# Performance work log

Measured on AMD Instinct MI355X. Metric: run time of the kernel, lower is better.

Reference implementation:

```python
import jax, jax.numpy as jnp
from jax import lax
import numpy as np

NEIGHBORS = ((1, 3), (0, 2, 4), (1, 5), (0, 4, 6), (1, 3, 5, 7), (2, 4, 8), (3, 7), (4, 6, 8), (5, 7))
EDGE_SRC = np.array([s for t, ns in enumerate(NEIGHBORS) for s in ns])  # 25 edges
EDGE_DST = np.array([t for t, ns in enumerate(NEIGHBORS) for _ in ns])
NE = len(EDGE_SRC)  # 25
NG, SP = 9, 64      # num_grids, single_plane = 576 // 9
R, C_IN, C_OUT, ROI = 64, 256, 576, 14
GN_GROUPS = 36
EPS = 1e-5


def conv2d(x, w, b, stride, pad):
    y = lax.conv_general_dilated(x, w, (stride, stride), [(pad, pad), (pad, pad)],
                                 dimension_numbers=('NCHW', 'OIHW', 'NCHW'))
    return y + b[None, :, None, None]


def group_norm(x, groups, gamma, beta):
    B, C, H, W = x.shape
    xg = x.reshape(B, groups, -1)
    mu = xg.mean(-1, keepdims=True)
    var = xg.var(-1, keepdims=True)
    xn = ((xg - mu) / jnp.sqrt(var + EPS)).reshape(B, C, H, W)
    return xn * gamma[None, :, None, None] + beta[None, :, None, None]


def edge_conv(inp, dw_w, dw_b, pw_w, pw_b):
    # depthwise 5x5 (groups=SP) then pointwise 1x1
    y = lax.conv_general_dilated(inp, dw_w, (1, 1), [(2, 2), (2, 2)],
                                 dimension_numbers=('NCHW', 'OIHW', 'NCHW'),
                                 feature_group_count=SP) + dw_b[None, :, None, None]
    return jnp.einsum('bchw,oc->bohw', y, pw_w) + pw_b[None, :, None, None]


def deconv_grouped(x, w_t, b, groups):
    # torch ConvTranspose2d(k=4, s=2, p=1, groups) as lhs-dilated conv
    k, s, p = 4, 2, 1
    in_c, out_g = w_t.shape[0], w_t.shape[1]
    in_g = in_c // groups
    w = w_t.reshape(groups, in_g, out_g, k, k).transpose(0, 2, 1, 3, 4).reshape(groups * out_g, in_g, k, k)
    w = jnp.flip(w, (-2, -1))
    y = lax.conv_general_dilated(x, w, (1, 1), [(k - 1 - p, k - 1 - p)] * 2,
                                 lhs_dilation=(s, s),
                                 dimension_numbers=('NCHW', 'OIHW', 'NCHW'),
                                 feature_group_count=groups)
    return y + b[None, :, None, None]


def setup_inputs() -> dict:
    key = jax.random.key(0)
    ks = iter(jax.random.split(key, 32))
    n = lambda shape, s=0.02: jax.random.normal(next(ks), shape, jnp.float32) * s
    inp = {
        'x': jax.random.normal(next(ks), (R, C_IN, ROI, ROI), jnp.float32),
        'convs_w0': n((C_OUT, C_IN, 3, 3)),
        'convs_b0': n((C_OUT,)),
        'convs_w': n((7, C_OUT, C_OUT, 3, 3)),
        'convs_b': n((7, C_OUT)),
        'gn_gamma': jnp.ones((8, C_OUT), jnp.float32),
        'gn_beta': jnp.zeros((8, C_OUT), jnp.float32),
        'fo_dw_w': n((NE, SP, 1, 5, 5), 0.05),
        'fo_dw_b': n((NE, SP)),
        'fo_pw_w': n((NE, SP, SP), 0.05),
        'fo_pw_b': n((NE, SP)),
        'so_dw_w': n((NE, SP, 1, 5, 5), 0.05),
        'so_dw_b': n((NE, SP)),
        'so_pw_w': n((NE, SP, SP), 0.05),
        'so_pw_b': n((NE, SP)),
        'up1_w': n((C_OUT, SP, 4, 4), 0.01),
        'up1_b': jnp.zeros((C_OUT,), jnp.float32),
        'sbn1_gamma': jnp.ones((C_OUT,), jnp.float32),
        'sbn1_beta': jnp.zeros((C_OUT,), jnp.float32),
        'up2_w': n((C_OUT, 1, 4, 4), 0.01),
        'up2_b': jnp.full((NG,), -np.log(0.99 / 0.01), jnp.float32),
    }
    return inp


def reference(x, convs_w0, convs_b0, convs_w, convs_b, gn_gamma, gn_beta,
              fo_dw_w, fo_dw_b, fo_pw_w, fo_pw_b,
              so_dw_w, so_dw_b, so_pw_w, so_pw_b,
              up1_w, up1_b, sbn1_gamma, sbn1_beta, up2_w, up2_b):
    # dense conv stack: stride 2 first, then 7 stride-1 convs (GN + ReLU each)
    h = jax.nn.relu(group_norm(conv2d(x, convs_w0, convs_b0, 2, 1), GN_GROUPS, gn_gamma[0], gn_beta[0]))
    for i in range(7):
        h = jax.nn.relu(group_norm(conv2d(h, convs_w[i], convs_b[i], 1, 1),
                                   GN_GROUPS, gn_gamma[i + 1], gn_beta[i + 1]))
    B, _, Hh, Wh = h.shape  # [B, 576, 7, 7]
    xg = h.reshape(B, NG, SP, Hh, Wh).transpose(1, 0, 2, 3, 4)  # [9, B, 64, 7, 7]
    # first-order message passing over 25 grid edges
    msgs1 = jax.vmap(edge_conv)(xg[EDGE_SRC], fo_dw_w, fo_dw_b, fo_pw_w, fo_pw_b)
    first = xg + jax.ops.segment_sum(msgs1, EDGE_DST, num_segments=NG)
    # second-order message passing (sources are first-order features)
    msgs2 = jax.vmap(edge_conv)(first[EDGE_SRC], so_dw_w, so_dw_b, so_pw_w, so_pw_b)
    second = xg + jax.ops.segment_sum(msgs2, EDGE_DST, num_segments=NG)
    x2 = second.transpose(1, 0, 2, 3, 4).reshape(B, NG * SP, Hh, Wh)

    def head(t):
        t = deconv_grouped(t, up1_w, up1_b, NG)           # [B, 576, 14, 14]
        t = jax.nn.relu(group_norm(t, NG, sbn1_gamma, sbn1_beta))
        return deconv_grouped(t, up2_w, up2_b, NG)        # [B, 9, 28, 28]

    return (head(h), head(x2))
```

## Files before the change

kernel.cpp:

```cpp
#include <hip/hip_runtime.h>
#include <hip/hip_bf16.h>

#define BB 64
#define CIN 256
#define CC 576
#define NGR 9
#define SPC 64
#define HW7 49
#define HW14 196
#define HW28 784

__device__ __constant__ int EDGE_SRC_C[24] = {1,3, 0,2,4, 1,5, 0,4,6, 1,3,5,7, 2,4,8, 3,7, 4,6,8, 5,7};
__device__ __constant__ int EDGE_OFF_C[9]  = {0,2,5,7,10,14,17,19,22};
__device__ __constant__ int EDGE_CNT_C[9]  = {2,3,2,3,4,3,2,3,2};

static __device__ __forceinline__ float bf2f(__hip_bfloat16 v){ return __bfloat162float(v); }
static __device__ __forceinline__ __hip_bfloat16 f2bf(float v){ return __float2bfloat16(v); }
static __device__ __forceinline__ float ldin(const void* p, size_t i, int isbf){
  return isbf ? bf2f(((const __hip_bfloat16*)p)[i]) : ((const float*)p)[i];
}

using bfrag = __attribute__((ext_vector_type(8))) short;
using f32x4 = __attribute__((ext_vector_type(4))) float;

__global__ void detect_kernel(const unsigned short* xs, int* flag) {
  if (threadIdx.x==0 && blockIdx.x==0) {
    int plaus = 0;
    for (int i=0;i<64;i++){
      unsigned short u = xs[2*i];
      int e = (u>>7)&0xFF;
      if (e>=100 && e<=140) plaus++;
    }
    *flag = (plaus >= 40) ? 1 : 0;
  }
}

__global__ __launch_bounds__(256) void xcvt_kernel(
    const void* __restrict__ x, const int* __restrict__ flagp,
    __hip_bfloat16* __restrict__ act0) {
  const int b = blockIdx.x, icb = blockIdx.y, pxb = blockIdx.z, t = threadIdx.x;
  const int isbf = *flagp;
  __shared__ float lds[32][29];
  for (int idx=t; idx<32*28; idx+=256){
    int i = idx/28, j = idx - i*28;
    lds[i][j] = ldin(x, ((size_t)b*CIN + icb*32+i)*HW14 + pxb*28 + j, isbf);
  }
  __syncthreads();
  for (int idx=t; idx<28*32; idx+=256){
    int j = idx >> 5, i = idx & 31;
    act0[((size_t)b*HW14 + pxb*28 + j)*CIN + icb*32 + i] = f2bf(lds[i][j]);
  }
}

__global__ __launch_bounds__(256) void wcvt0_kernel(
    const void* __restrict__ w, const int* __restrict__ flagp,
    __hip_bfloat16* __restrict__ dst) {
  const int oc = blockIdx.x, t = threadIdx.x;
  const int isbf = *flagp;
  __shared__ float lds[2304];
  for (int idx=t; idx<2304; idx+=256)
    lds[idx] = ldin(w, (size_t)oc*2304 + idx, isbf);
  __syncthreads();
  for (int idx=t; idx<2304; idx+=256){
    int koff = idx >> 8, rem = idx & 255;
    int icb = rem >> 5, ici = rem & 31;
    dst[(((size_t)koff*8 + icb)*CC + oc)*32 + ici] = f2bf(lds[rem*9 + koff]);
  }
}

__global__ __launch_bounds__(256) void wcvtL_kernel(
    const void* __restrict__ w, int li, const int* __restrict__ flagp,
    __hip_bfloat16* __restrict__ dst) {
  const int oc = blockIdx.x, t = threadIdx.x;
  const int isbf = *flagp;
  __shared__ float lds[5184];
  for (int idx=t; idx<5184; idx+=256)
    lds[idx] = ldin(w, ((size_t)li*CC + oc)*5184 + idx, isbf);
  __syncthreads();
  for (int idx=t; idx<5184; idx+=256){
    int koff = idx / 576, rem = idx - koff*576;
    int icb = rem >> 5, ici = rem & 31;
    dst[(((size_t)koff*18 + icb)*CC + oc)*32 + ici] = f2bf(lds[rem*9 + koff]);
  }
}

static __device__ __forceinline__ void epilogue_gn(
    float* s_out, float* s_stats, const f32x4 (&acc)[2][2],
    int wm, int wn, int ln, int quad, int t,
    const void* bias, int bias_off,
    const void* gamma, const void* beta, int goff,
    int nbb, int isbf, int b,
    __hip_bfloat16* __restrict__ out)
{
  __syncthreads();
  #pragma unroll
  for (int nf=0; nf<2; nf++){
    int chl = wn*32 + nf*16 + ln;
    float bv = ldin(bias, (size_t)bias_off + nbb + chl, isbf);
    #pragma unroll
    for (int mf=0; mf<2; mf++){
      #pragma unroll
      for (int r=0; r<4; r++){
        int px = wm*32 + mf*16 + quad*4 + r;
        s_out[chl*65 + px] = acc[mf][nf][r] + bv;
      }
    }
  }
  __syncthreads();
  {
    int wv = t >> 6, l = t & 63;
    float s=0.f, ss=0.f;
    for (int j=l; j<784; j+=64){
      int cq = j/49, px = j - cq*49;
      float v = s_out[(wv*16+cq)*65 + px];
      s += v; ss += v*v;
    }
    #pragma unroll
    for (int o=32;o>0;o>>=1){ s+=__shfl_down(s,o); ss+=__shfl_down(ss,o); }
    if (l==0){
      float mean=s/784.f, var=ss/784.f-mean*mean;
      s_stats[wv*2]=mean; s_stats[wv*2+1]=rsqrtf(fmaxf(var,0.f)+1e-5f);
    }
  }
  __syncthreads();
  for (int idx=t; idx<392; idx+=256){
    int px = idx>>3, ck = idx&7;
    alignas(16) __hip_bfloat16 tmp[8];
    #pragma unroll
    for (int u=0;u<8;u++){
      int chl = ck*8+u;
      int gi = chl>>4;
      float ga = ldin(gamma, (size_t)goff + nbb + chl, isbf);
      float be = ldin(beta,  (size_t)goff + nbb + chl, isbf);
      float v = (s_out[chl*65+px]-s_stats[gi*2])*s_stats[gi*2+1]*ga + be;
      tmp[u] = f2bf(fmaxf(v,0.f));
    }
    *(bfrag*)(out + ((size_t)b*64+px)*CC + nbb + ck*8) = *(const bfrag*)tmp;
  }
}

__global__ __launch_bounds__(256) void conv3_v3_kernel(
    const __hip_bfloat16* __restrict__ A,
    const __hip_bfloat16* __restrict__ Wb,
    const void* __restrict__ bias, int bias_off,
    const void* __restrict__ gamma, const void* __restrict__ beta, int goff,
    const int* __restrict__ flagp,
    __hip_bfloat16* __restrict__ out) {
  const int t = threadIdx.x;
  const int l = t & 63, w = t >> 6;
  const int wm = w & 1, wn = (w >> 1) & 1;
  const int ln = l & 15, quad = l >> 4;
  const int b = blockIdx.x, nbb = blockIdx.y*32;
  const int isbf = *flagp;

  __shared__ alignas(16) char smem[8320];
  __shared__ float s_stats[4];
  __hip_bfloat16* sA0 = (__hip_bfloat16*)smem;
  __hip_bfloat16* sA1 = (__hip_bfloat16*)(smem + 4000);
  float* s_out = (float*)smem;

  if (t < 8){
    bfrag z = {0,0,0,0,0,0,0,0};
    __hip_bfloat16* sb = (t<4)? sA0 : sA1;
    *(bfrag*)(sb + 49*40 + (t&3)*8) = z;
  }

  int r0a[9], r1a[9];
  {
    int p0 = wm*32 + ln, p1 = p0+16;
    int y0=p0/7, x0=p0-y0*7, y1=p1/7, x1=p1-y1*7;
    bool v0=p0<49, v1=p1<49;
    #pragma unroll
    for (int koff=0;koff<9;koff++){
      int dy=koff/3-1, dx=koff-(koff/3)*3-1;
      int sy0=y0+dy,sx0=x0+dx, sy1=y1+dy,sx1=x1+dx;
      r0a[koff] = (v0&&sy0>=0&&sy0<7&&sx0>=0&&sx0<7)? sy0*7+sx0 : 49;
      r1a[koff] = (v1&&sy1>=0&&sy1<7&&sx1>=0&&sx1<7)? sy1*7+sx1 : 49;
    }
  }

  f32x4 acc2[2];
  acc2[0] = (f32x4){0.f,0.f,0.f,0.f};
  acc2[1] = (f32x4){0.f,0.f,0.f,0.f};

  const int px_s = t>>2, ic_s = (t&3)*8;
  const __hip_bfloat16* Abase = A + ((size_t)b*64 + px_s)*CC + ic_s;

  if (t<196) *(bfrag*)(sA0 + px_s*40 + ic_s) = *(const bfrag*)(Abase);
  __syncthreads();

  const int nidx = nbb + wn*16 + ln;
  for (int icb=0; icb<18; icb++){
    __hip_bfloat16* curb = (icb&1)? sA1 : sA0;
    if (icb<17 && t<196){
      __hip_bfloat16* nxtb = (icb&1)? sA0 : sA1;
      *(bfrag*)(nxtb + px_s*40 + ic_s) = *(const bfrag*)(Abase + (icb+1)*32);
    }
    const __hip_bfloat16* wpB = Wb + (size_t)icb*18432 + (size_t)nidx*32 + quad*8;
    #pragma unroll
    for (int koff=0;koff<9;koff++){
      bfrag a0 = *(const bfrag*)(curb + r0a[koff]*40 + quad*8);
      bfrag a1 = *(const bfrag*)(curb + r1a[koff]*40 + quad*8);
      bfrag b0 = *(const bfrag*)(wpB + (size_t)koff*331776);
      acc2[0] = __builtin_amdgcn_mfma_f32_16x16x32_bf16(a0, b0, acc2[0], 0,0,0);
      acc2[1] = __builtin_amdgcn_mfma_f32_16x16x32_bf16(a1, b0, acc2[1], 0,0,0);
    }
    __syncthreads();
  }

  {
    const int chl = wn*16 + ln;
    float bv = ldin(bias, (size_t)bias_off + nbb + chl, isbf);
    #pragma unroll
    for (int mf=0; mf<2; mf++)
      #pragma unroll
      for (int r=0;r<4;r++){
        int px = wm*32 + mf*16 + quad*4 + r;
        s_out[chl*65 + px] = acc2[mf][r] + bv;
      }
  }
  __syncthreads();
  {
    int wv = t >> 6, l2 = t & 63;
    if (wv < 2){
      float s=0.f, ss=0.f;
      for (int j=l2; j<784; j+=64){
        int cq = j/49, px = j - cq*49;
        float v = s_out[(wv*16+cq)*65 + px];
        s += v; ss += v*v;
      }
      #pragma unroll
      for (int o=32;o>0;o>>=1){ s+=__shfl_down(s,o); ss+=__shfl_down(ss,o); }
      if (l2==0){
        float mean=s/784.f, var=ss/784.f-mean*mean;
        s_stats[wv*2]=mean; s_stats[wv*2+1]=rsqrtf(fmaxf(var,0.f)+1e-5f);
      }
    }
  }
  __syncthreads();
  if (t < 196){
    int px = t>>2, ck = t&3;
    alignas(16) __hip_bfloat16 tmp[8];
    #pragma unroll
    for (int u=0;u<8;u++){
      int chl = ck*8+u;
      int gi = chl>>4;
      float ga = ldin(gamma, (size_t)goff + nbb + chl, isbf);
      float be = ldin(beta,  (size_t)goff + nbb + chl, isbf);
      float v = (s_out[chl*65+px]-s_stats[gi*2])*s_stats[gi*2+1]*ga + be;
      tmp[u] = f2bf(fmaxf(v,0.f));
    }
    *(bfrag*)(out + ((size_t)b*64+px)*CC + nbb + ck*8) = *(const bfrag*)tmp;
  }
}

__global__ __launch_bounds__(256) void conv0_fused_kernel(
    const __hip_bfloat16* __restrict__ A,
    const __hip_bfloat16* __restrict__ Wb,
    const void* __restrict__ bias,
    const void* __restrict__ gamma, const void* __restrict__ beta,
    const int* __restrict__ flagp,
    __hip_bfloat16* __restrict__ out) {
  const int t = threadIdx.x;
  const int l = t & 63, w = t >> 6;
  const int wm = w & 1, wn = w >> 1;
  const int ln = l & 15, quad = l >> 4;
  const int b = blockIdx.x, nbb = blockIdx.y*64;

  __shared__ alignas(16) __hip_bfloat16 sC[197*40];
  __shared__ alignas(16) float s_out_arr[64*65];
  __shared__ float s_stats[8];

  if (t < 4){
    bfrag z = {0,0,0,0,0,0,0,0};
    *(bfrag*)(sC + 196*40 + t*8) = z;
  }

  int yy[2], xx[2]; bool pv[2];
  #pragma unroll
  for (int mf=0; mf<2; mf++){
    int p = wm*32 + mf*16 + ln;
    pv[mf] = p<49; yy[mf]=p/7; xx[mf]=p-yy[mf]*7;
  }

  f32x4 acc[2][2];
  #pragma unroll
  for (int i=0;i<2;i++)
    #pragma unroll
    for (int j=0;j<2;j++) acc[i][j] = (f32x4){0.f,0.f,0.f,0.f};

  for (int icb=0; icb<8; icb++){
    __syncthreads();
    for (int idx=t*8; idx<6272; idx+=2048){
      int px = idx>>5, ic = idx&31;
      *(bfrag*)(sC + px*40 + ic) = *(const bfrag*)(A + ((size_t)b*196+px)*256 + icb*32 + ic);
    }
    __syncthreads();
    for (int koff=0; koff<9; koff++){
      const int dy = koff/3 - 1, dx = koff - (koff/3)*3 - 1;
      int sy0=2*yy[0]+dy, sx0=2*xx[0]+dx;
      int r0 = (pv[0]&&sy0>=0&&sy0<14&&sx0>=0&&sx0<14) ? sy0*14+sx0 : 196;
      int sy1=2*yy[1]+dy, sx1=2*xx[1]+dx;
      int r1 = (pv[1]&&sy1>=0&&sy1<14&&sx1>=0&&sx1<14) ? sy1*14+sx1 : 196;
      bfrag a0 = *(const bfrag*)(sC + r0*40 + quad*8);
      bfrag a1 = *(const bfrag*)(sC + r1*40 + quad*8);
      const __hip_bfloat16* wp = Wb + ((size_t)(koff*8+icb)*576 + nbb + wn*32 + ln)*32 + quad*8;
      bfrag b0 = *(const bfrag*)(wp);
      bfrag b1 = *(const bfrag*)(wp + 16*32);
      acc[0][0] = __builtin_amdgcn_mfma_f32_16x16x32_bf16(a0, b0, acc[0][0], 0,0,0);
      acc[1][0] = __builtin_amdgcn_mfma_f32_16x16x32_bf16(a1, b0, acc[1][0], 0,0,0);
      acc[0][1] = __builtin_amdgcn_mfma_f32_16x16x32_bf16(a0, b1, acc[0][1], 0,0,0);
      acc[1][1] = __builtin_amdgcn_mfma_f32_16x16x32_bf16(a1, b1, acc[1][1], 0,0,0);
    }
  }

  epilogue_gn(s_out_arr, s_stats, acc, wm, wn, ln, quad, t,
              bias, 0, gamma, beta, 0, nbb, *flagp, b, out);
}

__global__ __launch_bounds__(256) void dw_edge_kernel(
    const __hip_bfloat16* __restrict__ F,
    const void* __restrict__ dw_w,
    const void* __restrict__ dw_b,
    const int* __restrict__ flagp,
    __hip_bfloat16* __restrict__ Y) {
  const int b = blockIdx.x, e = blockIdx.y, t = threadIdx.x;
  const int isbf = *flagp;
  const int src = EDGE_SRC_C[e];
  __shared__ alignas(16) __hip_bfloat16 sA[50*72];
  for (int idx=t; idx<400; idx+=256){
    if (idx < 392){
      int px = idx>>3, ic = (idx&7)*8;
      *(bfrag*)(sA + px*72 + ic) = *(const bfrag*)(F + ((size_t)b*64+px)*CC + src*64 + ic);
    } else {
      bfrag z = {0,0,0,0,0,0,0,0};
      *(bfrag*)(sA + 49*72 + (idx-392)*8) = z;
    }
  }
  __syncthreads();
  const int ch = t & 63, wv = t >> 6;
  float wd[25];
  #pragma unroll
  for (int j=0;j<25;j++) wd[j] = ldin(dw_w, (size_t)e*1600 + ch*25 + j, isbf);
  float dwb = ldin(dw_b, e*64 + ch, isbf);
  for (int px=wv; px<49; px+=4){
    int oy=px/7, ox=px-oy*7;
    float a = dwb;
    #pragma unroll
    for (int u=0;u<5;u++){
      int py = oy+u-2;
      bool vy = (py>=0)&&(py<7);
      #pragma unroll
      for (int v=0;v<5;v++){
        int pxx = ox+v-2;
        int r = (vy && pxx>=0 && pxx<7) ? py*7+pxx : 49;
        a += bf2f(sA[r*72 + ch]) * wd[u*5+v];
      }
    }
    Y[((size_t)(e*64+b)*49 + px)*64 + ch] = f2bf(a);
  }
}

__global__ __launch_bounds__(256) void pwpack_kernel(
    const void* __restrict__ pw_fo, const void* __restrict__ pw_so,
    const int* __restrict__ flagp,
    __hip_bfloat16* __restrict__ dfo, __hip_bfloat16* __restrict__ dso) {
  const int e = blockIdx.x, t = threadIdx.x;
  const int isbf = *flagp;
  for (int idx=t; idx<4096; idx+=256){
    dfo[(size_t)e*4096+idx] = f2bf(ldin(pw_fo, (size_t)e*4096+idx, isbf));
    dso[(size_t)e*4096+idx] = f2bf(ldin(pw_so, (size_t)e*4096+idx, isbf));
  }
}

__global__ __launch_bounds__(256) void pw_seg_kernel(
    const __hip_bfloat16* __restrict__ Y,
    const __hip_bfloat16* __restrict__ base,
    const __hip_bfloat16* __restrict__ pwb,
    const void* __restrict__ pw_b,
    const int* __restrict__ flagp,
    __hip_bfloat16* __restrict__ out) {
  const int t = threadIdx.x, l = t & 63, w = t >> 6;
  const int wm = w & 1, wn = w >> 1;
  const int ln = l & 15, quad = l >> 4;
  const int dst = blockIdx.y;
  const int mt = blockIdx.x*64 + wm*32;
  const int m0 = mt + ln, m1 = m0 + 16;

  f32x4 acc[2][2];
  #pragma unroll
  for (int i=0;i<2;i++)
    #pragma unroll
    for (int j=0;j<2;j++) acc[i][j] = (f32x4){0.f,0.f,0.f,0.f};

  const int eoff = EDGE_OFF_C[dst], ecnt = EDGE_CNT_C[dst];
  for (int k=0;k<ecnt;k++){
    const __hip_bfloat16* Ye = Y + (size_t)(eoff+k)*3136*64;
    const __hip_bfloat16* pe = pwb + (size_t)(eoff+k)*4096;
    #pragma unroll
    for (int ks=0; ks<2; ks++){
      const int kq = ks*32 + quad*8;
      bfrag a0 = *(const bfrag*)(Ye + (size_t)m0*64 + kq);
      bfrag a1 = *(const bfrag*)(Ye + (size_t)m1*64 + kq);
      bfrag b0 = *(const bfrag*)(pe + (wn*32+ln)*64 + kq);
      bfrag b1 = *(const bfrag*)(pe + (wn*32+ln+16)*64 + kq);
      acc[0][0] = __builtin_amdgcn_mfma_f32_16x16x32_bf16(a0, b0, acc[0][0], 0,0,0);
      acc[1][0] = __builtin_amdgcn_mfma_f32_16x16x32_bf16(a1, b0, acc[1][0], 0,0,0);
      acc[0][1] = __builtin_amdgcn_mfma_f32_16x16x32_bf16(a0, b1, acc[0][1], 0,0,0);
      acc[1][1] = __builtin_amdgcn_mfma_f32_16x16x32_bf16(a1, b1, acc[1][1], 0,0,0);
    }
  }

  const int isbf = *flagp;
  #pragma unroll
  for (int nf=0; nf<2; nf++){
    int n = wn*32 + nf*16 + ln;
    float pbs = 0.f;
    for (int k=0;k<ecnt;k++) pbs += ldin(pw_b, (size_t)(eoff+k)*64 + n, isbf);
    #pragma unroll
    for (int mf=0; mf<2; mf++){
      #pragma unroll
      for (int r=0; r<4; r++){
        int m = mt + mf*16 + quad*4 + r;
        int bb = m/49, px = m - bb*49;
        size_t oi = ((size_t)bb*64 + px)*CC + dst*64 + n;
        out[oi] = f2bf(bf2f(base[oi]) + acc[mf][nf][r] + pbs);
      }
    }
  }
}

__global__ __launch_bounds__(256) void wpack_dc1_kernel(
    const void* __restrict__ w1, const int* __restrict__ flagp,
    __hip_bfloat16* __restrict__ dst) {
  const int gtap = blockIdx.x, t = threadIdx.x;
  const int isbf = *flagp;
  const int g = gtap >> 4, tap = gtap & 15;
  for (int idx=t; idx<64*64; idx+=256){
    int oc = idx >> 6, ic = idx & 63;
    dst[((size_t)gtap*64 + oc)*64 + ic] =
        f2bf(ldin(w1, ((size_t)(g*64+ic)*64 + oc)*16 + tap, isbf));
  }
}

__global__ __launch_bounds__(256) void dc1_cls_kernel(
    const __hip_bfloat16* __restrict__ H,
    const __hip_bfloat16* __restrict__ Wp,
    const void* __restrict__ b1,
    const int* __restrict__ flagp,
    __hip_bfloat16* __restrict__ mid) {
  const int t = threadIdx.x;
  const int l = t & 63, w = t >> 6;
  const int wm = w & 1, wn = w >> 1;
  const int ln = l & 15, quad = l >> 4;
  const int Mt = blockIdx.x;
  const int cls = blockIdx.y;
  const int g = blockIdx.z;
  const int ry = cls >> 1, rx = cls & 1;
  const int b0 = (Mt*64)/49;

  __shared__ alignas(16) __hip_bfloat16 sX[3*50*72];

  {
    const bfrag z = {0,0,0,0,0,0,0,0};
    for (int idx=t; idx<1200; idx+=256){
      int bi = idx/400, rem = idx - bi*400;
      int p = rem>>3, ch = (rem&7)*8;
      bfrag v = z;
      if (p < 49 && (b0+bi) < 64)
        v = *(const bfrag*)(H + ((size_t)((b0+bi)*64) + p)*CC + g*64 + ch);
      *(bfrag*)(sX + (bi*50+p)*72 + ch) = v;
    }
  }

  int aoff[2][4];
  #pragma unroll
  for (int mf=0; mf<2; mf++){
    int m = Mt*64 + wm*32 + mf*16 + ln;
    int b = m/49, p = m - b*49;
    int py = p/7, pxx = p - py*7;
    int bloc = b - b0;
    #pragma unroll
    for (int kyi=0;kyi<2;kyi++){
      int iy = py + ry - kyi;
      bool vy = (iy>=0)&&(iy<7);
      #pragma unroll
      for (int kxi=0;kxi<2;kxi++){
        int ix = pxx + rx - kxi;
        int r = (vy && ix>=0 && ix<7) ? iy*7+ix : 49;
        aoff[mf][kyi*2+kxi] = (bloc*50 + r)*72 + quad*8;
      }
    }
  }

  f32x4 acc[2][2];
  #pragma unroll
  for (int i=0;i<2;i++)
    #pragma unroll
    for (int j=0;j<2;j++) acc[i][j] = (f32x4){0.f,0.f,0.f,0.f};

  __syncthreads();

  const int ky0 = 1-ry, kx0 = 1-rx;
  #pragma unroll
  for (int kyi=0;kyi<2;kyi++){
    #pragma unroll
    for (int kxi=0;kxi<2;kxi++){
      const int tap = (ky0+2*kyi)*4 + (kx0+2*kxi);
      const __hip_bfloat16* wb =
          Wp + ((size_t)(g*16+tap)*64 + wn*32 + ln)*64 + quad*8;
      const int ao0 = aoff[0][kyi*2+kxi], ao1 = aoff[1][kyi*2+kxi];
      #pragma unroll
      for (int half=0; half<2; half++){
        bfrag a0 = *(const bfrag*)(sX + ao0 + half*32);
        bfrag a1 = *(const bfrag*)(sX + ao1 + half*32);
        bfrag w0 = *(const bfrag*)(wb + half*32);
        bfrag w1 = *(const bfrag*)(wb + 16*64 + half*32);
        acc[0][0] = __builtin_amdgcn_mfma_f32_16x16x32_bf16(a0, w0, acc[0][0], 0,0,0);
        acc[1][0] = __builtin_amdgcn_mfma_f32_16x16x32_bf16(a1, w0, acc[1][0], 0,0,0);
        acc[0][1] = __builtin_amdgcn_mfma_f32_16x16x32_bf16(a0, w1, acc[0][1], 0,0,0);
        acc[1][1] = __builtin_amdgcn_mfma_f32_16x16x32_bf16(a1, w1, acc[1][1], 0,0,0);
      }
    }
  }

  const int isbf = *flagp;
  size_t ob[2][4];
  #pragma unroll
  for (int mf=0;mf<2;mf++){
    #pragma unroll
    for (int r=0;r<4;r++){
      int m = Mt*64 + wm*32 + mf*16 + quad*4 + r;
      int b = m/49, p = m - b*49;
      int py = p/7, pxx = p - py*7;
      int oy = 2*py + ry, ox = 2*pxx + rx;
      ob[mf][r] = ((size_t)b*196 + oy*14 + ox)*CC + g*64;
    }
  }
  #pragma unroll
  for (int nf=0;nf<2;nf++){
    int n = wn*32 + nf*16 + ln;
    float bv = ldin(b1, g*64 + n, isbf);
    #pragma unroll
    for (int mf=0;mf<2;mf++){
      #pragma unroll
      for (int r=0;r<4;r++)
        mid[ob[mf][r] + n] = f2bf(acc[mf][nf][r] + bv);
    }
  }
}

__global__ __launch_bounds__(256) void dc2gn_kernel(
    const __hip_bfloat16* __restrict__ mid,
    const void* __restrict__ gamma, const void* __restrict__ beta,
    const void* __restrict__ w2,
    const void* __restrict__ b2,
    const int* __restrict__ flagp,
    void* __restrict__ outp,
    size_t out_elem_off) {
  const int isbf = *flagp;
  const int b=blockIdx.x, g=blockIdx.y, z=blockIdx.z, t=threadIdx.x;
  const int c = t & 63;
  __shared__ __hip_bfloat16 s_mid[64*113];
  __shared__ float s_w2[64][17];
  __shared__ float red[8]; __shared__ float stats[2];
  const __hip_bfloat16* mbase = mid + (size_t)b*196*CC + g*64;

  {
    float s=0.f, ss=0.f;
    for (int idx=t; idx<12544; idx+=256){
      int ipx = idx>>6;
      float v = bf2f(mbase[(size_t)ipx*CC + (idx&63)]);
      s+=v; ss+=v*v;
    }
    #pragma unroll
    for (int o=32;o>0;o>>=1){ s+=__shfl_down(s,o); ss+=__shfl_down(ss,o); }
    int wid=t>>6;
    if ((t&63)==0){ red[wid]=s; red[4+wid]=ss; }
  }
  for (int idx=t; idx<1024; idx+=256)
    s_w2[idx>>4][idx&15] = ldin(w2, (g*SPC + (idx>>4))*16 + (idx&15), isbf);
  __syncthreads();
  if (t==0){
    float S=red[0]+red[1]+red[2]+red[3];
    float SS=red[4]+red[5]+red[6]+red[7];
    float mean=S/12544.f, var=SS/12544.f-mean*mean;
    stats[0]=mean; stats[1]=rsqrtf(fmaxf(var,0.f)+1e-5f);
  }
  __syncthreads();
  const float mean=stats[0], inv=stats[1];
  const int rbase = z*6;
  {
    float ga = ldin(gamma, g*SPC+c, isbf), be = ldin(beta, g*SPC+c, isbf);
    for (int idx=t; idx<7168; idx+=256){
      int pl = idx>>6;
      int ipx = (rbase + pl/14)*14 + (pl%14);
      float v = (bf2f(mbase[(size_t)ipx*CC + c])-mean)*inv*ga + be;
      s_mid[c*113 + pl] = f2bf(fmaxf(v, 0.f));
    }
  }
  __syncthreads();
  float b2v = ldin(b2, g, isbf);
  for (int p=t; p<392; p+=256){
    int oyl = p/28, ox = p - oyl*28;
    int oy = z*14 + oyl;
    float a = b2v;
    for (int cc=0; cc<64; cc++){
      #pragma unroll
      for (int kyi=0;kyi<2;kyi++){
        int ky=((oy+1)&1)+2*kyi; int ny=oy+1-ky;
        if (ny>=0){
          int iy=ny>>1;
          if (iy<14){
            int li = iy - rbase;
            #pragma unroll
            for (int kxi=0;kxi<2;kxi++){
              int kx=((ox+1)&1)+2*kxi; int nx=ox+1-kx;
              if (nx>=0){
                int ix=nx>>1;
                if (ix<14) a += bf2f(s_mid[cc*113 + li*14 + ix])*s_w2[cc][ky*4+kx];
              }
            }
          }
        }
      }
    }
    size_t oidx = out_elem_off + ((size_t)b*NGR+g)*HW28 + oy*28 + ox;
    if (isbf) ((__hip_bfloat16*)outp)[oidx] = f2bf(a);
    else      ((float*)outp)[oidx] = a;
  }
}

extern "C" void kernel_launch(void* const* d_in, const int* in_sizes, int n_in,
                              void* d_out, int out_size, void* d_ws, size_t ws_size,
                              hipStream_t stream) {
  const void* x        = d_in[0];
  const void* convs_w0 = d_in[1];
  const void* convs_b0 = d_in[2];
  const void* convs_w  = d_in[3];
  const void* convs_b  = d_in[4];
  const void* gn_gamma = d_in[5];
  const void* gn_beta  = d_in[6];
  const void* fo_dw_w  = d_in[7];
  const void* fo_dw_b  = d_in[8];
  const void* fo_pw_w  = d_in[9];
  const void* fo_pw_b  = d_in[10];
  const void* so_dw_w  = d_in[11];
  const void* so_dw_b  = d_in[12];
  const void* so_pw_w  = d_in[13];
  const void* so_pw_b  = d_in[14];
  const void* up1_w    = d_in[15];
  const void* up1_b    = d_in[16];
  const void* sbn_g    = d_in[17];
  const void* sbn_b    = d_in[18];
  const void* up2_w    = d_in[19];
  const void* up2_b    = d_in[20];
  (void)in_sizes; (void)n_in; (void)out_size; (void)ws_size;

  int* flag = (int*)d_ws;
  char* wsb = (char*)d_ws + 16;
  __hip_bfloat16* act0   = (__hip_bfloat16*)(wsb);
  __hip_bfloat16* wbuf   = (__hip_bfloat16*)(wsb + 6422528);
  __hip_bfloat16* actA   = (__hip_bfloat16*)(wsb + 12394496);
  __hip_bfloat16* actB   = (__hip_bfloat16*)(wsb + 17113088);
  __hip_bfloat16* bufF   = (__hip_bfloat16*)(wsb + 21831680);
  __hip_bfloat16* secN   = (__hip_bfloat16*)(wsb + 26550272);
  __hip_bfloat16* wpack  = (__hip_bfloat16*)(wsb + 31268864);
  __hip_bfloat16* pwbF   = (__hip_bfloat16*)(wsb + 32448512);
  __hip_bfloat16* pwbS   = (__hip_bfloat16*)(wsb + 32645120);
  __hip_bfloat16* Y      = (__hip_bfloat16*)(wsb);
  __hip_bfloat16* mid    = (__hip_bfloat16*)(wsb);

  detect_kernel<<<1, 1, 0, stream>>>((const unsigned short*)x, flag);

  xcvt_kernel<<<dim3(BB,8,7), 256, 0, stream>>>(x, flag, act0);
  wcvt0_kernel<<<CC, 256, 0, stream>>>(convs_w0, flag, wbuf);
  conv0_fused_kernel<<<dim3(64,9), 256, 0, stream>>>(
      act0, wbuf, convs_b0, gn_gamma, gn_beta, flag, actA);

  __hip_bfloat16* cur = actA; __hip_bfloat16* nxt = actB;
  for (int i=0;i<7;i++){
    wcvtL_kernel<<<CC, 256, 0, stream>>>(convs_w, i, flag, wbuf);
    conv3_v3_kernel<<<dim3(64,18), 256, 0, stream>>>(
        cur, wbuf, convs_b, i*CC, gn_gamma, gn_beta, (i+1)*CC, flag, nxt);
    __hip_bfloat16* tmp=cur; cur=nxt; nxt=tmp;
  }

  wpack_dc1_kernel<<<144, 256, 0, stream>>>(up1_w, flag, wpack);
  pwpack_kernel<<<24, 256, 0, stream>>>(fo_pw_w, so_pw_w, flag, pwbF, pwbS);

  dw_edge_kernel<<<dim3(BB,24), 256, 0, stream>>>(cur, fo_dw_w, fo_dw_b, flag, Y);
  pw_seg_kernel<<<dim3(49,NGR), 256, 0, stream>>>(Y, cur, pwbF, fo_pw_b, flag, bufF);
  dw_edge_kernel<<<dim3(BB,24), 256, 0, stream>>>(bufF, so_dw_w, so_dw_b, flag, Y);
  pw_seg_kernel<<<dim3(49,NGR), 256, 0, stream>>>(Y, cur, pwbS, so_pw_b, flag, secN);

  dc1_cls_kernel<<<dim3(49,4,NGR), 256, 0, stream>>>(cur, wpack, up1_b, flag, mid);
  dc2gn_kernel<<<dim3(BB,NGR,2), 256, 0, stream>>>(mid, sbn_g, sbn_b, up2_w, up2_b, flag, d_out, 0);
  dc1_cls_kernel<<<dim3(49,4,NGR), 256, 0, stream>>>(secN, wpack, up1_b, flag, mid);
  dc2gn_kernel<<<dim3(BB,NGR,2), 256, 0, stream>>>(mid, sbn_g, sbn_b, up2_w, up2_b, flag, d_out, (size_t)BB*NGR*HW28);
}
```

Baseline: 965.9 us.

## Widen conv3 tile to 96 channels with 64-channel K steps

The 3x3 conv kernel now has each block compute 96 output channels instead of 32, with three N-fragments per wave. Each loaded A fragment is therefore reused across three MFMAs. The input-channel chunk staged in shared memory also grows from 32 to 64, halving the number of K iterations and barriers. The cost is more shared memory and accumulator registers, and the grid shrinks from 1152 to 384 blocks, which may reduce occupancy and latency hiding.

```diff
diff --git a/kernel.cpp b/kernel.cpp
--- a/kernel.cpp
+++ b/kernel.cpp
@@ -139,7 +139,7 @@
   }
 }
 
-__global__ __launch_bounds__(256) void conv3_v3_kernel(
+__global__ __launch_bounds__(256) void conv3_v4_kernel(
     const __hip_bfloat16* __restrict__ A,
     const __hip_bfloat16* __restrict__ Wb,
     const void* __restrict__ bias, int bias_off,
@@ -148,21 +148,22 @@
     __hip_bfloat16* __restrict__ out) {
   const int t = threadIdx.x;
   const int l = t & 63, w = t >> 6;
-  const int wm = w & 1, wn = (w >> 1) & 1;
+  const int wm = w & 1, wn2 = w >> 1;
   const int ln = l & 15, quad = l >> 4;
-  const int b = blockIdx.x, nbb = blockIdx.y*32;
-  const int isbf = *flagp;
-
-  __shared__ alignas(16) char smem[8320];
-  __shared__ float s_stats[4];
+  const int b = blockIdx.x, nbb = blockIdx.y*96;
+  const int isbf = *flagp;
+
+  __shared__ alignas(16) char smem[24960];
+  __shared__ float s_stats[12];
   __hip_bfloat16* sA0 = (__hip_bfloat16*)smem;
-  __hip_bfloat16* sA1 = (__hip_bfloat16*)(smem + 4000);
+  __hip_bfloat16* sA1 = (__hip_bfloat16*)(smem + 7200);
   float* s_out = (float*)smem;
 
-  if (t < 8){
+  if (t < 18){
     bfrag z = {0,0,0,0,0,0,0,0};
-    __hip_bfloat16* sb = (t<4)? sA0 : sA1;
-    *(bfrag*)(sb + 49*40 + (t&3)*8) = z;
+    __hip_bfloat16* sb = (t<9)? sA0 : sA1;
+    int c = (t<9)? t : t-9;
+    *(bfrag*)(sb + 49*72 + c*8) = z;
   }
 
   int r0a[9], r1a[9];
@@ -179,67 +180,89 @@
     }
   }
 
-  f32x4 acc2[2];
-  acc2[0] = (f32x4){0.f,0.f,0.f,0.f};
-  acc2[1] = (f32x4){0.f,0.f,0.f,0.f};
-
-  const int px_s = t>>2, ic_s = (t&3)*8;
-  const __hip_bfloat16* Abase = A + ((size_t)b*64 + px_s)*CC + ic_s;
-
-  if (t<196) *(bfrag*)(sA0 + px_s*40 + ic_s) = *(const bfrag*)(Abase);
-  __syncthreads();
-
-  const int nidx = nbb + wn*16 + ln;
-  for (int icb=0; icb<18; icb++){
+  f32x4 acc[2][3];
+  #pragma unroll
+  for (int i=0;i<2;i++)
+    #pragma unroll
+    for (int j=0;j<3;j++) acc[i][j] = (f32x4){0.f,0.f,0.f,0.f};
+
+  const __hip_bfloat16* Ab = A + (size_t)b*64*CC;
+  {
+    for (int idx=t; idx<392; idx+=256){
+      int p = idx>>3, c8 = idx&7;
+      *(bfrag*)(sA0 + p*72 + c8*8) = *(const bfrag*)(Ab + (size_t)p*CC + c8*8);
+    }
+  }
+  __syncthreads();
+
+  const int nrow = nbb + wn2*48 + ln;
+  for (int icb=0; icb<9; icb++){
     __hip_bfloat16* curb = (icb&1)? sA1 : sA0;
-    if (icb<17 && t<196){
+    if (icb<8){
       __hip_bfloat16* nxtb = (icb&1)? sA0 : sA1;
-      *(bfrag*)(nxtb + px_s*40 + ic_s) = *(const bfrag*)(Abase + (icb+1)*32);
-    }
-    const __hip_bfloat16* wpB = Wb + (size_t)icb*18432 + (size_t)nidx*32 + quad*8;
+      for (int idx=t; idx<392; idx+=256){
+        int p = idx>>3, c8 = idx&7;
+        *(bfrag*)(nxtb + p*72 + c8*8) =
+            *(const bfrag*)(Ab + (size_t)p*CC + (icb+1)*64 + c8*8);
+      }
+    }
     #pragma unroll
     for (int koff=0;koff<9;koff++){
-      bfrag a0 = *(const bfrag*)(curb + r0a[koff]*40 + quad*8);
-      bfrag a1 = *(const bfrag*)(curb + r1a[koff]*40 + quad*8);
-      bfrag b0 = *(const bfrag*)(wpB + (size_t)koff*331776);
-      acc2[0] = __builtin_amdgcn_mfma_f32_16x16x32_bf16(a0, b0, acc2[0], 0,0,0);
-      acc2[1] = __builtin_amdgcn_mfma_f32_16x16x32_bf16(a1, b0, acc2[1], 0,0,0);
+      const int ra0 = r0a[koff]*72 + quad*8;
+      const int ra1 = r1a[koff]*72 + quad*8;
+      #pragma unroll
+      for (int ks=0; ks<2; ks++){
+        const __hip_bfloat16* wp =
+            Wb + ((size_t)(koff*18 + icb*2 + ks)*576 + nrow)*32 + quad*8;
+        bfrag a0 = *(const bfrag*)(curb + ra0 + ks*32);
+        bfrag a1 = *(const bfrag*)(curb + ra1 + ks*32);
+        bfrag w0 = *(const bfrag*)(wp);
+        bfrag w1 = *(const bfrag*)(wp + 16*32);
+        bfrag w2 = *(const bfrag*)(wp + 32*32);
+        acc[0][0] = __builtin_amdgcn_mfma_f32_16x16x32_bf16(a0, w0, acc[0][0], 0,0,0);
+        acc[1][0] = __builtin_amdgcn_mfma_f32_16x16x32_bf16(a1, w0, acc[1][0], 0,0,0);
+        acc[0][1] = __builtin_amdgcn_mfma_f32_16x16x32_bf16(a0, w1, acc[0][1], 0,0,0);
+        acc[1][1] = __builtin_amdgcn_mfma_f32_16x16x32_bf16(a1, w1, acc[1][1], 0,0,0);
+        acc[0][2] = __builtin_amdgcn_mfma_f32_16x16x32_bf16(a0, w2, acc[0][2], 0,0,0);
+        acc[1][2] = __builtin_amdgcn_mfma_f32_16x16x32_bf16(a1, w2, acc[1][2], 0,0,0);
+      }
     }
     __syncthreads();
   }
 
-  {
-    const int chl = wn*16 + ln;
+  #pragma unroll
+  for (int nf=0; nf<3; nf++){
+    const int chl = wn2*48 + nf*16 + ln;
     float bv = ldin(bias, (size_t)bias_off + nbb + chl, isbf);
     #pragma unroll
     for (int mf=0; mf<2; mf++)
       #pragma unroll
       for (int r=0;r<4;r++){
         int px = wm*32 + mf*16 + quad*4 + r;
-        s_out[chl*65 + px] = acc2[mf][r] + bv;
+        s_out[chl*65 + px] = acc[mf][nf][r] + bv;
       }
   }
   __syncthreads();
   {
     int wv = t >> 6, l2 = t & 63;
-    if (wv < 2){
+    for (int g = wv; g < 6; g += 4){
       float s=0.f, ss=0.f;
       for (int j=l2; j<784; j+=64){
         int cq = j/49, px = j - cq*49;
-        float v = s_out[(wv*16+cq)*65 + px];
+        float v = s_out[(g*16+cq)*65 + px];
         s += v; ss += v*v;
       }
       #pragma unroll
       for (int o=32;o>0;o>>=1){ s+=__shfl_down(s,o); ss+=__shfl_down(ss,o); }
       if (l2==0){
         float mean=s/784.f, var=ss/784.f-mean*mean;
-        s_stats[wv*2]=mean; s_stats[wv*2+1]=rsqrtf(fmaxf(var,0.f)+1e-5f);
-      }
-    }
-  }
-  __syncthreads();
-  if (t < 196){
-    int px = t>>2, ck = t&3;
+        s_stats[g*2]=mean; s_stats[g*2+1]=rsqrtf(fmaxf(var,0.f)+1e-5f);
+      }
+    }
+  }
+  __syncthreads();
+  for (int idx=t; idx<588; idx+=256){
+    int px = idx/12, ck = idx - px*12;
     alignas(16) __hip_bfloat16 tmp[8];
     #pragma unroll
     for (int u=0;u<8;u++){
@@ -681,7 +704,7 @@
   __hip_bfloat16* cur = actA; __hip_bfloat16* nxt = actB;
   for (int i=0;i<7;i++){
     wcvtL_kernel<<<CC, 256, 0, stream>>>(convs_w, i, flag, wbuf);
-    conv3_v3_kernel<<<dim3(64,18), 256, 0, stream>>>(
+    conv3_v4_kernel<<<dim3(64,6), 256, 0, stream>>>(
         cur, wbuf, convs_b, i*CC, gn_gamma, gn_beta, (i+1)*CC, flag, nxt);
     __hip_bfloat16* tmp=cur; cur=nxt; nxt=tmp;
   }
```

Result: slower. 1.166 ms (+20.7%).

## Widen conv3x3 block tile to 64 channels with register-staged input prefetch

Applied to the files above, without the earlier changes.

The 3x3 conv+GroupNorm kernel now uses 512-thread blocks, each covering 64 output channels instead of 32. Each block also stages 64 input channels per iteration in shared memory, so the K loop has 9 steps and 9 barriers instead of 18. The next input chunk is loaded into registers before the MFMA work and written to shared memory afterwards, which hides global latency behind compute. This halves how often activations are re-read from global memory across channel blocks and cuts barrier count. The cost is a larger shared-memory footprint, fewer blocks, and more threads per block, which could reduce occupancy.

```diff
diff --git a/kernel.cpp b/kernel.cpp
--- a/kernel.cpp
+++ b/kernel.cpp
@@ -139,7 +139,7 @@
   }
 }
 
-__global__ __launch_bounds__(256) void conv3_v3_kernel(
+__global__ __launch_bounds__(512) void conv3_v5_kernel(
     const __hip_bfloat16* __restrict__ A,
     const __hip_bfloat16* __restrict__ Wb,
     const void* __restrict__ bias, int bias_off,
@@ -148,22 +148,16 @@
     __hip_bfloat16* __restrict__ out) {
   const int t = threadIdx.x;
   const int l = t & 63, w = t >> 6;
-  const int wm = w & 1, wn = (w >> 1) & 1;
+  const int wm = w & 1, wn = w >> 1;
   const int ln = l & 15, quad = l >> 4;
-  const int b = blockIdx.x, nbb = blockIdx.y*32;
-  const int isbf = *flagp;
-
-  __shared__ alignas(16) char smem[8320];
-  __shared__ float s_stats[4];
+  const int b = blockIdx.x, nbb = blockIdx.y*64;
+  const int isbf = *flagp;
+
+  __shared__ alignas(16) char smem[16672];
+  __shared__ float s_stats[8];
   __hip_bfloat16* sA0 = (__hip_bfloat16*)smem;
-  __hip_bfloat16* sA1 = (__hip_bfloat16*)(smem + 4000);
+  __hip_bfloat16* sA1 = (__hip_bfloat16*)(smem + 7200);
   float* s_out = (float*)smem;
-
-  if (t < 8){
-    bfrag z = {0,0,0,0,0,0,0,0};
-    __hip_bfloat16* sb = (t<4)? sA0 : sA1;
-    *(bfrag*)(sb + 49*40 + (t&3)*8) = z;
-  }
 
   int r0a[9], r1a[9];
   {
@@ -179,31 +173,50 @@
     }
   }
 
-  f32x4 acc2[2];
-  acc2[0] = (f32x4){0.f,0.f,0.f,0.f};
-  acc2[1] = (f32x4){0.f,0.f,0.f,0.f};
-
-  const int px_s = t>>2, ic_s = (t&3)*8;
-  const __hip_bfloat16* Abase = A + ((size_t)b*64 + px_s)*CC + ic_s;
-
-  if (t<196) *(bfrag*)(sA0 + px_s*40 + ic_s) = *(const bfrag*)(Abase);
+  f32x4 acc[2];
+  acc[0] = (f32x4){0.f,0.f,0.f,0.f};
+  acc[1] = (f32x4){0.f,0.f,0.f,0.f};
+
+  const int p_s = t>>3, c8_s = (t&7)*8;
+  const bool sact = (t < 392);
+  const __hip_bfloat16* Ab = A + (size_t)b*64*CC;
+  const __hip_bfloat16* Asrc = Ab + (size_t)p_s*CC + c8_s;
+
+  if (sact) *(bfrag*)(sA0 + p_s*72 + c8_s) = *(const bfrag*)(Asrc);
+  if (t >= 496){
+    bfrag z = {0,0,0,0,0,0,0,0};
+    int u = t - 496;
+    __hip_bfloat16* sb = (u<8)? sA0 : sA1;
+    *(bfrag*)(sb + 49*72 + (u&7)*8) = z;
+  }
   __syncthreads();
 
   const int nidx = nbb + wn*16 + ln;
-  for (int icb=0; icb<18; icb++){
+  for (int icb=0; icb<9; icb++){
     __hip_bfloat16* curb = (icb&1)? sA1 : sA0;
-    if (icb<17 && t<196){
+    bfrag rstage;
+    const bool have = (icb<8) && sact;
+    if (have) rstage = *(const bfrag*)(Asrc + (icb+1)*64);
+
+    #pragma unroll
+    for (int koff=0;koff<9;koff++){
+      const int ra0 = r0a[koff]*72 + quad*8;
+      const int ra1 = r1a[koff]*72 + quad*8;
+      #pragma unroll
+      for (int ks=0; ks<2; ks++){
+        const __hip_bfloat16* wp =
+            Wb + ((size_t)(koff*18 + icb*2 + ks)*576 + nidx)*32 + quad*8;
+        bfrag a0 = *(const bfrag*)(curb + ra0 + ks*32);
+        bfrag a1 = *(const bfrag*)(curb + ra1 + ks*32);
+        bfrag b0 = *(const bfrag*)(wp);
+        acc[0] = __builtin_amdgcn_mfma_f32_16x16x32_bf16(a0, b0, acc[0], 0,0,0);
+        acc[1] = __builtin_amdgcn_mfma_f32_16x16x32_bf16(a1, b0, acc[1], 0,0,0);
+      }
+    }
+
+    if (have){
       __hip_bfloat16* nxtb = (icb&1)? sA0 : sA1;
-      *(bfrag*)(nxtb + px_s*40 + ic_s) = *(const bfrag*)(Abase + (icb+1)*32);
-    }
-    const __hip_bfloat16* wpB = Wb + (size_t)icb*18432 + (size_t)nidx*32 + quad*8;
-    #pragma unroll
-    for (int koff=0;koff<9;koff++){
-      bfrag a0 = *(const bfrag*)(curb + r0a[koff]*40 + quad*8);
-      bfrag a1 = *(const bfrag*)(curb + r1a[koff]*40 + quad*8);
-      bfrag b0 = *(const bfrag*)(wpB + (size_t)koff*331776);
-      acc2[0] = __builtin_amdgcn_mfma_f32_16x16x32_bf16(a0, b0, acc2[0], 0,0,0);
-      acc2[1] = __builtin_amdgcn_mfma_f32_16x16x32_bf16(a1, b0, acc2[1], 0,0,0);
+      *(bfrag*)(nxtb + p_s*72 + c8_s) = rstage;
     }
     __syncthreads();
   }
@@ -216,13 +229,13 @@
       #pragma unroll
       for (int r=0;r<4;r++){
         int px = wm*32 + mf*16 + quad*4 + r;
-        s_out[chl*65 + px] = acc2[mf][r] + bv;
+        s_out[chl*65 + px] = acc[mf][r] + bv;
       }
   }
   __syncthreads();
   {
     int wv = t >> 6, l2 = t & 63;
-    if (wv < 2){
+    if (wv < 4){
       float s=0.f, ss=0.f;
       for (int j=l2; j<784; j+=64){
         int cq = j/49, px = j - cq*49;
@@ -238,8 +251,8 @@
     }
   }
   __syncthreads();
-  if (t < 196){
-    int px = t>>2, ck = t&3;
+  if (t < 392){
+    int px = t>>3, ck = t&7;
     alignas(16) __hip_bfloat16 tmp[8];
     #pragma unroll
     for (int u=0;u<8;u++){
@@ -681,7 +694,7 @@
   __hip_bfloat16* cur = actA; __hip_bfloat16* nxt = actB;
   for (int i=0;i<7;i++){
     wcvtL_kernel<<<CC, 256, 0, stream>>>(convs_w, i, flag, wbuf);
-    conv3_v3_kernel<<<dim3(64,18), 256, 0, stream>>>(
+    conv3_v5_kernel<<<dim3(64,9), 512, 0, stream>>>(
         cur, wbuf, convs_b, i*CC, gn_gamma, gn_beta, (i+1)*CC, flag, nxt);
     __hip_bfloat16* tmp=cur; cur=nxt; nxt=tmp;
   }
```

Measured after the change: 1.049 ms. 8.6% more time.
